# Performance work log

Hardware: AMD Instinct MI355X
Metric: run time of the kernel (lower is better)

Reference implementation:

```python
import jax, jax.numpy as jnp
import numpy as np

B, R, T = 32, 256, 4096  # shots, receivers, time samples; P = T prob grid
EPS = 1e-8


def _trapz(y, t):
    # trapezoidal integral along last axis
    dt = t[1:] - t[:-1]
    return jnp.sum(0.5 * (y[..., 1:] + y[..., :-1]) * dt, axis=-1)


def _cum_trap(y, t):
    # cumulative trapezoid along last axis, prepend 0 -> same length as y
    dt = t[1:] - t[:-1]
    incr = 0.5 * (y[..., 1:] + y[..., :-1]) * dt
    c = jnp.cumsum(incr, axis=-1)
    return jnp.concatenate([jnp.zeros_like(c[..., :1]), c], axis=-1)


def _renorm(x, t):
    # square + trapz-normalize each trace to a probability density over t
    pdf = x * x + EPS
    return pdf / _trapz(pdf, t)[..., None]


def setup_inputs() -> dict:
    key = jax.random.key(0)
    k1, k2 = jax.random.split(key)
    traces = 0.5 * jax.random.normal(k1, (B, R, T), dtype=jnp.float32)
    t = jnp.arange(T, dtype=jnp.float32) * 1e-3
    p = jnp.linspace(0.0, 1.0, T, dtype=jnp.float32)  # probability grid
    # q_raw = true_quantile(obs_data, t, p): invert the observed CDF per trace
    obs = 0.5 * jax.random.normal(k2, (B, R, T), dtype=jnp.float32)
    obs_pdf = _renorm(obs, t)
    obs_cdf = _cum_trap(obs_pdf, t)  # strictly increasing (pdf > 0)
    q_raw = jax.vmap(lambda c: jnp.interp(p, c, t))(obs_cdf.reshape(-1, T))
    q_raw = q_raw.reshape(B, R, T).astype(jnp.float32)
    return {"traces": traces, "t": t, "p": p, "q_raw": q_raw}


def reference(traces, t, p, q_raw):
    pdf = _renorm(traces, t)          # [B,R,T]
    cdf = _cum_trap(pdf, t)           # [B,R,T], in [0,1]
    # quantile lookup: interpolate each trace's quantile table at its cdf values
    cdf_f = cdf.reshape(-1, T)
    q_f = q_raw.reshape(-1, T)
    transport = jax.vmap(jnp.interp, in_axes=(0, None, 0))(cdf_f, p, q_f)
    transport = transport.reshape(pdf.shape)
    diff = t - transport
    loss = jnp.sum(_trapz(diff * diff * pdf, t))
    return loss
```

## Files before the change

### kernel.cpp

```cpp
#include <hip/hip_runtime.h>

#define TT 4096
#define BLK 256
#define PER 16
#define EPSV 1e-8f

__global__ __launch_bounds__(BLK) void w2_loss_kernel(
    const float* __restrict__ traces,
    const float* __restrict__ q_raw,
    float* __restrict__ part) {
  __shared__ float lds_q[TT];
  __shared__ float wave_sums[4];
  __shared__ float wave_red[4];

  const int tid = threadIdx.x;
  const long trace = blockIdx.x;
  const float* __restrict__ tr = traces + trace * TT;
  const float* __restrict__ qr = q_raw + trace * TT;

  const int base = tid * PER;

  float4 trv[4];
  {
    const float4* tr4 = (const float4*)(tr + base);
#pragma unroll
    for (int j = 0; j < 4; ++j) trv[j] = tr4[j];
  }
  float nb = (base + PER < TT) ? tr[base + PER] : 0.0f;

  {
    const float4* q4 = (const float4*)qr;
    float4* lq4 = (float4*)lds_q;
#pragma unroll
    for (int j = 0; j < 4; ++j) lq4[tid + BLK * j] = q4[tid + BLK * j];
  }

  float s[PER + 1];
#pragma unroll
  for (int j = 0; j < 4; ++j) {
    s[4 * j + 0] = trv[j].x * trv[j].x + EPSV;
    s[4 * j + 1] = trv[j].y * trv[j].y + EPSV;
    s[4 * j + 2] = trv[j].z * trv[j].z + EPSV;
    s[4 * j + 3] = trv[j].w * trv[j].w + EPSV;
  }
  s[PER] = (base + PER < TT) ? (nb * nb + EPSV) : 0.0f;

  float lc[PER + 1];
  lc[0] = 0.0f;
#pragma unroll
  for (int m = 0; m < PER; ++m) {
    float t0 = (float)(base + m) * 1e-3f;
    float t1 = (float)(base + m + 1) * 1e-3f;
    float incr = (base + m < TT - 1) ? 0.5f * (s[m] + s[m + 1]) * (t1 - t0)
                                     : 0.0f;
    lc[m + 1] = lc[m] + incr;
  }
  const float tot = lc[PER];

  float v = tot;
#pragma unroll
  for (int off = 1; off < 64; off <<= 1) {
    float n = __shfl_up(v, off, 64);
    if ((tid & 63) >= off) v += n;
  }
  if ((tid & 63) == 63) wave_sums[tid >> 6] = v;
  __syncthreads();

  const int wv = tid >> 6;
  float wave_off = 0.0f;
  if (wv > 0) wave_off += wave_sums[0];
  if (wv > 1) wave_off += wave_sums[1];
  if (wv > 2) wave_off += wave_sums[2];
  const float excl = (v - tot) + wave_off;
  const float norm = wave_sums[0] + wave_sums[1] + wave_sums[2] + wave_sums[3];
  const float inv_norm = 1.0f / norm;

  float local = 0.0f;
#pragma unroll
  for (int m = 0; m < PER; ++m) {
    float x = (excl + lc[m]) * inv_norm;
    float u = x * (float)(TT - 1);
    int i0 = (int)floorf(u);
    i0 = (i0 < 0) ? 0 : ((i0 > TT - 2) ? TT - 2 : i0);
    float f = u - (float)i0;
    f = fminf(fmaxf(f, 0.0f), 1.0f);
    float q0 = lds_q[i0];
    float q1 = lds_q[i0 + 1];
    float transport = q0 + f * (q1 - q0);
    float tm = (float)(base + m) * 1e-3f;
    float d = tm - transport;
    float tlo = (float)((base + m == 0) ? 0 : (base + m - 1)) * 1e-3f;
    float thi = (float)((base + m == TT - 1) ? (TT - 1) : (base + m + 1)) * 1e-3f;
    float w = 0.5f * (thi - tlo);
    local += d * d * s[m] * w;
  }
  local *= inv_norm;

#pragma unroll
  for (int off = 32; off > 0; off >>= 1) local += __shfl_down(local, off, 64);
  if ((tid & 63) == 0) wave_red[tid >> 6] = local;
  __syncthreads();
  if (tid == 0) {
    part[blockIdx.x] = wave_red[0] + wave_red[1] + wave_red[2] + wave_red[3];
  }
}

__global__ __launch_bounds__(BLK) void reduce_kernel(
    const float* __restrict__ part, float* __restrict__ out, int n) {
  __shared__ float wave_red[4];
  const int tid = threadIdx.x;
  float local = 0.0f;
  for (int i = tid; i < n; i += BLK) local += part[i];
#pragma unroll
  for (int off = 32; off > 0; off >>= 1) local += __shfl_down(local, off, 64);
  if ((tid & 63) == 0) wave_red[tid >> 6] = local;
  __syncthreads();
  if (tid == 0) out[0] = wave_red[0] + wave_red[1] + wave_red[2] + wave_red[3];
}

extern "C" void kernel_launch(void* const* d_in, const int* in_sizes, int n_in,
                              void* d_out, int out_size, void* d_ws, size_t ws_size,
                              hipStream_t stream) {
  const float* traces = (const float*)d_in[0];
  const float* q_raw  = (const float*)d_in[3];
  float* out = (float*)d_out;
  float* part = (float*)d_ws;

  const int n_traces = in_sizes[0] / TT;
  w2_loss_kernel<<<n_traces, BLK, 0, stream>>>(traces, q_raw, part);
  reduce_kernel<<<1, BLK, 0, stream>>>(part, out, n_traces);
}
```

Before: 283.8 us.

## Transpose interpolation through swizzled LDS and gather quantile table from global memory

Stops staging the full quantile table in LDS. Each thread's partial CDF values are written to a swizzled LDS buffer and re-read in element-major order, so adjacent lanes handle adjacent samples and their q_raw gathers hit nearby global/cache addresses. The squared differences are written back through the same buffer and reduced in the original per-thread layout. Occupancy is also hinted with launch_bounds(BLK, 8). The cost is an extra LDS round trip and barrier, and the quantile lookups now go through L1/L2 instead of LDS.

```diff
diff --git a/kernel.cpp b/kernel.cpp
--- a/kernel.cpp
+++ b/kernel.cpp
@@ -5,18 +5,23 @@
 #define PER 16
 #define EPSV 1e-8f
 
-__global__ __launch_bounds__(BLK) void w2_loss_kernel(
+__device__ __forceinline__ int swz(int i) {
+  return i ^ (((i >> 5) & 7) << 2);
+}
+
+__global__ __launch_bounds__(BLK, 8) void w2_loss_kernel(
     const float* __restrict__ traces,
     const float* __restrict__ q_raw,
     float* __restrict__ part) {
-  __shared__ float lds_q[TT];
+  __shared__ float lds_buf[TT];
+  __shared__ float lds_wexcl[BLK];
   __shared__ float wave_sums[4];
   __shared__ float wave_red[4];
 
   const int tid = threadIdx.x;
   const long trace = blockIdx.x;
-  const float* __restrict__ tr = traces + trace * TT;
-  const float* __restrict__ qr = q_raw + trace * TT;
+  const float* __restrict__ tr = traces + trace * (long)TT;
+  const float* __restrict__ qr = q_raw + trace * (long)TT;
 
   const int base = tid * PER;
 
@@ -27,13 +32,6 @@
     for (int j = 0; j < 4; ++j) trv[j] = tr4[j];
   }
   float nb = (base + PER < TT) ? tr[base + PER] : 0.0f;
-
-  {
-    const float4* q4 = (const float4*)qr;
-    float4* lq4 = (float4*)lds_q;
-#pragma unroll
-    for (int j = 0; j < 4; ++j) lq4[tid + BLK * j] = q4[tid + BLK * j];
-  }
 
   float s[PER + 1];
 #pragma unroll
@@ -64,35 +62,70 @@
     if ((tid & 63) >= off) v += n;
   }
   if ((tid & 63) == 63) wave_sums[tid >> 6] = v;
+
+  lds_wexcl[tid] = v - tot;
+
+  const int swb = ((tid >> 1) & 7) << 2;
+#pragma unroll
+  for (int j = 0; j < 4; ++j) {
+    *(float4*)&lds_buf[(base + 4 * j) ^ swb] =
+        make_float4(lc[4 * j + 0], lc[4 * j + 1], lc[4 * j + 2], lc[4 * j + 3]);
+  }
   __syncthreads();
 
-  const int wv = tid >> 6;
-  float wave_off = 0.0f;
-  if (wv > 0) wave_off += wave_sums[0];
-  if (wv > 1) wave_off += wave_sums[1];
-  if (wv > 2) wave_off += wave_sums[2];
-  const float excl = (v - tot) + wave_off;
-  const float norm = wave_sums[0] + wave_sums[1] + wave_sums[2] + wave_sums[3];
+  const float ws0 = wave_sums[0], ws1 = wave_sums[1];
+  const float ws2 = wave_sums[2], ws3 = wave_sums[3];
+  const float norm = ws0 + ws1 + ws2 + ws3;
   const float inv_norm = 1.0f / norm;
+
+  const float woff1 = ws0;
+  const float woff2 = ws0 + ws1;
+  const float woff3 = (ws0 + ws1) + ws2;
+
+#pragma unroll
+  for (int g = 0; g < 4; ++g) {
+    const float woff = (g == 0) ? 0.0f : ((g == 1) ? woff1 : ((g == 2) ? woff2 : woff3));
+#pragma unroll
+    for (int mm = 0; mm < 4; ++mm) {
+      const int m = 4 * g + mm;
+      const int e = (m << 8) + tid;
+      const int a = swz(e);
+      const float lcv = lds_buf[a];
+      const float wex = lds_wexcl[e >> 4];
+      const float excl = wex + woff;
+      const float x = (excl + lcv) * inv_norm;
+      float u = x * (float)(TT - 1);
+      int i0 = (int)floorf(u);
+      i0 = (i0 < 0) ? 0 : ((i0 > TT - 2) ? TT - 2 : i0);
+      float f = u - (float)i0;
+      f = fminf(fmaxf(f, 0.0f), 1.0f);
+      const float q0 = qr[i0];
+      const float q1 = qr[i0 + 1];
+      const float transport = q0 + f * (q1 - q0);
+      const float tm = (float)e * 1e-3f;
+      const float d = tm - transport;
+      lds_buf[a] = d * d;
+    }
+  }
+  __syncthreads();
+
+  float dd[PER];
+#pragma unroll
+  for (int j = 0; j < 4; ++j) {
+    const float4 dq = *(const float4*)&lds_buf[(base + 4 * j) ^ swb];
+    dd[4 * j + 0] = dq.x;
+    dd[4 * j + 1] = dq.y;
+    dd[4 * j + 2] = dq.z;
+    dd[4 * j + 3] = dq.w;
+  }
 
   float local = 0.0f;
 #pragma unroll
   for (int m = 0; m < PER; ++m) {
-    float x = (excl + lc[m]) * inv_norm;
-    float u = x * (float)(TT - 1);
-    int i0 = (int)floorf(u);
-    i0 = (i0 < 0) ? 0 : ((i0 > TT - 2) ? TT - 2 : i0);
-    float f = u - (float)i0;
-    f = fminf(fmaxf(f, 0.0f), 1.0f);
-    float q0 = lds_q[i0];
-    float q1 = lds_q[i0 + 1];
-    float transport = q0 + f * (q1 - q0);
-    float tm = (float)(base + m) * 1e-3f;
-    float d = tm - transport;
     float tlo = (float)((base + m == 0) ? 0 : (base + m - 1)) * 1e-3f;
     float thi = (float)((base + m == TT - 1) ? (TT - 1) : (base + m + 1)) * 1e-3f;
     float w = 0.5f * (thi - tlo);
-    local += d * d * s[m] * w;
+    local += dd[m] * s[m] * w;
   }
   local *= inv_norm;
 
```

Result: no change. 287.5 us (+1.3%).

## Process eight traces per block with double-buffered async q_raw prefetch into LDS

Applied to the files above, without the earlier changes.

Each block now handles eight consecutive traces instead of one. While it computes the current trace, it prefetches the next trace's quantile table into a second LDS buffer using global_load_lds, and loads the next trace samples into registers. The goal is to hide global memory latency behind the scan and interpolation work and to cut per-block launch overhead. In exchange there are 8x fewer blocks and LDS use doubles. Correctness depends on the barrier waiting for the asynchronous LDS writes to finish.

```diff
diff --git a/kernel.cpp b/kernel.cpp
--- a/kernel.cpp
+++ b/kernel.cpp
@@ -3,105 +3,134 @@
 #define TT 4096
 #define BLK 256
 #define PER 16
+#define TPB 8
 #define EPSV 1e-8f
 
-__global__ __launch_bounds__(BLK) void w2_loss_kernel(
+__device__ __forceinline__ void async_q16(const float* __restrict__ g, float* l) {
+  __builtin_amdgcn_global_load_lds(
+      (const __attribute__((address_space(1))) void*)g,
+      (__attribute__((address_space(3))) void*)l,
+      16, 0, 0);
+}
+
+__global__ __launch_bounds__(BLK, 4) void w2_loss_kernel(
     const float* __restrict__ traces,
     const float* __restrict__ q_raw,
     float* __restrict__ part) {
-  __shared__ float lds_q[TT];
+  __shared__ float qb[2][TT];
   __shared__ float wave_sums[4];
   __shared__ float wave_red[4];
 
   const int tid = threadIdx.x;
-  const long trace = blockIdx.x;
-  const float* __restrict__ tr = traces + trace * TT;
-  const float* __restrict__ qr = q_raw + trace * TT;
-
+  const int wv = tid >> 6;
+  const int lane = tid & 63;
+  const long trace0 = (long)blockIdx.x * TPB;
   const int base = tid * PER;
 
+  {
+    const float* qr = q_raw + trace0 * (long)TT;
+#pragma unroll
+    for (int j = 0; j < 4; ++j) {
+      const int c = (wv * 4 + j) * 256;
+      async_q16(qr + c + lane * 4, &qb[0][c]);
+    }
+  }
   float4 trv[4];
+  float nb;
   {
+    const float* tr = traces + trace0 * (long)TT;
     const float4* tr4 = (const float4*)(tr + base);
 #pragma unroll
     for (int j = 0; j < 4; ++j) trv[j] = tr4[j];
-  }
-  float nb = (base + PER < TT) ? tr[base + PER] : 0.0f;
-
-  {
-    const float4* q4 = (const float4*)qr;
-    float4* lq4 = (float4*)lds_q;
-#pragma unroll
-    for (int j = 0; j < 4; ++j) lq4[tid + BLK * j] = q4[tid + BLK * j];
+    nb = (base + PER < TT) ? tr[base + PER] : 0.0f;
   }
 
-  float s[PER + 1];
+  for (int k = 0; k < TPB; ++k) {
+    const int buf = k & 1;
+    const long trace = trace0 + k;
+
+    float s[PER + 1];
 #pragma unroll
-  for (int j = 0; j < 4; ++j) {
-    s[4 * j + 0] = trv[j].x * trv[j].x + EPSV;
-    s[4 * j + 1] = trv[j].y * trv[j].y + EPSV;
-    s[4 * j + 2] = trv[j].z * trv[j].z + EPSV;
-    s[4 * j + 3] = trv[j].w * trv[j].w + EPSV;
-  }
-  s[PER] = (base + PER < TT) ? (nb * nb + EPSV) : 0.0f;
+    for (int j = 0; j < 4; ++j) {
+      s[4 * j + 0] = trv[j].x * trv[j].x + EPSV;
+      s[4 * j + 1] = trv[j].y * trv[j].y + EPSV;
+      s[4 * j + 2] = trv[j].z * trv[j].z + EPSV;
+      s[4 * j + 3] = trv[j].w * trv[j].w + EPSV;
+    }
+    s[PER] = (base + PER < TT) ? (nb * nb + EPSV) : 0.0f;
 
-  float lc[PER + 1];
-  lc[0] = 0.0f;
+    float lc[PER + 1];
+    lc[0] = 0.0f;
 #pragma unroll
-  for (int m = 0; m < PER; ++m) {
-    float t0 = (float)(base + m) * 1e-3f;
-    float t1 = (float)(base + m + 1) * 1e-3f;
-    float incr = (base + m < TT - 1) ? 0.5f * (s[m] + s[m + 1]) * (t1 - t0)
-                                     : 0.0f;
-    lc[m + 1] = lc[m] + incr;
-  }
-  const float tot = lc[PER];
+    for (int m = 0; m < PER; ++m) {
+      float t0 = (float)(base + m) * 1e-3f;
+      float t1 = (float)(base + m + 1) * 1e-3f;
+      float incr = (base + m < TT - 1) ? 0.5f * (s[m] + s[m + 1]) * (t1 - t0)
+                                       : 0.0f;
+      lc[m + 1] = lc[m] + incr;
+    }
+    const float tot = lc[PER];
 
-  float v = tot;
+    float v = tot;
 #pragma unroll
-  for (int off = 1; off < 64; off <<= 1) {
-    float n = __shfl_up(v, off, 64);
-    if ((tid & 63) >= off) v += n;
-  }
-  if ((tid & 63) == 63) wave_sums[tid >> 6] = v;
-  __syncthreads();
+    for (int off = 1; off < 64; off <<= 1) {
+      float n = __shfl_up(v, off, 64);
+      if (lane >= off) v += n;
+    }
+    if (lane == 63) wave_sums[wv] = v;
+    __syncthreads();
 
-  const int wv = tid >> 6;
-  float wave_off = 0.0f;
-  if (wv > 0) wave_off += wave_sums[0];
-  if (wv > 1) wave_off += wave_sums[1];
-  if (wv > 2) wave_off += wave_sums[2];
-  const float excl = (v - tot) + wave_off;
-  const float norm = wave_sums[0] + wave_sums[1] + wave_sums[2] + wave_sums[3];
-  const float inv_norm = 1.0f / norm;
+    if (k + 1 < TPB) {
+      const float* qr_n = q_raw + (trace + 1) * (long)TT;
+#pragma unroll
+      for (int j = 0; j < 4; ++j) {
+        const int c = (wv * 4 + j) * 256;
+        async_q16(qr_n + c + lane * 4, &qb[buf ^ 1][c]);
+      }
+      const float* tr_n = traces + (trace + 1) * (long)TT;
+      const float4* tr4_n = (const float4*)(tr_n + base);
+#pragma unroll
+      for (int j = 0; j < 4; ++j) trv[j] = tr4_n[j];
+      nb = (base + PER < TT) ? tr_n[base + PER] : 0.0f;
+    }
 
-  float local = 0.0f;
+    float wave_off = 0.0f;
+    if (wv > 0) wave_off += wave_sums[0];
+    if (wv > 1) wave_off += wave_sums[1];
+    if (wv > 2) wave_off += wave_sums[2];
+    const float excl = (v - tot) + wave_off;
+    const float norm = wave_sums[0] + wave_sums[1] + wave_sums[2] + wave_sums[3];
+    const float inv_norm = 1.0f / norm;
+
+    const float* __restrict__ lq = qb[buf];
+    float local = 0.0f;
 #pragma unroll
-  for (int m = 0; m < PER; ++m) {
-    float x = (excl + lc[m]) * inv_norm;
-    float u = x * (float)(TT - 1);
-    int i0 = (int)floorf(u);
-    i0 = (i0 < 0) ? 0 : ((i0 > TT - 2) ? TT - 2 : i0);
-    float f = u - (float)i0;
-    f = fminf(fmaxf(f, 0.0f), 1.0f);
-    float q0 = lds_q[i0];
-    float q1 = lds_q[i0 + 1];
-    float transport = q0 + f * (q1 - q0);
-    float tm = (float)(base + m) * 1e-3f;
-    float d = tm - transport;
-    float tlo = (float)((base + m == 0) ? 0 : (base + m - 1)) * 1e-3f;
-    float thi = (float)((base + m == TT - 1) ? (TT - 1) : (base + m + 1)) * 1e-3f;
-    float w = 0.5f * (thi - tlo);
-    local += d * d * s[m] * w;
-  }
-  local *= inv_norm;
+    for (int m = 0; m < PER; ++m) {
+      float x = (excl + lc[m]) * inv_norm;
+      float u = x * (float)(TT - 1);
+      int i0 = (int)floorf(u);
+      i0 = (i0 < 0) ? 0 : ((i0 > TT - 2) ? TT - 2 : i0);
+      float f = u - (float)i0;
+      f = fminf(fmaxf(f, 0.0f), 1.0f);
+      float q0 = lq[i0];
+      float q1 = lq[i0 + 1];
+      float transport = q0 + f * (q1 - q0);
+      float tm = (float)(base + m) * 1e-3f;
+      float d = tm - transport;
+      float tlo = (float)((base + m == 0) ? 0 : (base + m - 1)) * 1e-3f;
+      float thi = (float)((base + m == TT - 1) ? (TT - 1) : (base + m + 1)) * 1e-3f;
+      float w = 0.5f * (thi - tlo);
+      local += d * d * s[m] * w;
+    }
+    local *= inv_norm;
 
 #pragma unroll
-  for (int off = 32; off > 0; off >>= 1) local += __shfl_down(local, off, 64);
-  if ((tid & 63) == 0) wave_red[tid >> 6] = local;
-  __syncthreads();
-  if (tid == 0) {
-    part[blockIdx.x] = wave_red[0] + wave_red[1] + wave_red[2] + wave_red[3];
+    for (int off = 32; off > 0; off >>= 1) local += __shfl_down(local, off, 64);
+    if (lane == 0) wave_red[wv] = local;
+    __syncthreads();
+    if (tid == 0) {
+      part[trace] = wave_red[0] + wave_red[1] + wave_red[2] + wave_red[3];
+    }
   }
 }
 
@@ -127,6 +156,7 @@
   float* part = (float*)d_ws;
 
   const int n_traces = in_sizes[0] / TT;
-  w2_loss_kernel<<<n_traces, BLK, 0, stream>>>(traces, q_raw, part);
+  const int n_blocks = n_traces / TPB;
+  w2_loss_kernel<<<n_blocks, BLK, 0, stream>>>(traces, q_raw, part);
   reduce_kernel<<<1, BLK, 0, stream>>>(part, out, n_traces);
 }
```

Result: slower. 295.7 us (+4.2%).
